# Optimization experiments

Hardware: AMD Instinct MI355X
Metric: run time of the kernel (lower is better)

## Reference

```python
import jax, jax.numpy as jnp
import numpy as np

DIM, HEADS, WS, SHIFT = 192, 6, 8, 4
HEAD_DIM = DIM // HEADS
SCALE = HEAD_DIM ** -0.5
EPS = 1e-5


def _rel_pos_index(ws):
    coords = np.stack(np.meshgrid(np.arange(ws), np.arange(ws), indexing='ij'))  # [2,ws,ws]
    flat = coords.reshape(2, -1)
    rel = flat[:, :, None] - flat[:, None, :]          # [2,N,N]
    rel = rel.transpose(1, 2, 0)
    rel[:, :, 0] += ws - 1
    rel[:, :, 1] += ws - 1
    rel[:, :, 0] *= 2 * ws - 1
    return rel.sum(-1)                                  # [N,N] int


def _attn_mask(H, W, ws, shift):
    if shift == 0:
        return None
    img = np.zeros((H, W), dtype=np.float32)
    cnt = 0
    for hs in (slice(0, -ws), slice(-ws, -shift), slice(-shift, None)):
        for wsl in (slice(0, -ws), slice(-ws, -shift), slice(-shift, None)):
            img[hs, wsl] = cnt
            cnt += 1
    mw = img.reshape(H // ws, ws, W // ws, ws).transpose(0, 2, 1, 3).reshape(-1, ws * ws)  # [nW,N]
    m = mw[:, None, :] - mw[:, :, None]
    return jnp.asarray(np.where(m != 0, -100.0, 0.0).astype(np.float32))  # [nW,N,N]


def _ln(x, w, b):
    mu = x.mean(-1, keepdims=True)
    var = ((x - mu) ** 2).mean(-1, keepdims=True)
    return (x - mu) * jax.lax.rsqrt(var + EPS) * w + b


def setup_inputs() -> dict:
    key = jax.random.key(0)
    ks = jax.random.split(key, 10)
    B, H, W, C = 64, 56, 56, DIM
    hid = 4 * C
    p = lambda k, sh, s=0.02: jax.random.normal(k, sh, jnp.float32) * s
    return {
        'x': jax.random.normal(ks[0], (B, H * W, C), jnp.float32),
        'ln1_w': jnp.ones((C,), jnp.float32), 'ln1_b': jnp.zeros((C,), jnp.float32),
        'qkv_w': p(ks[1], (C, 3 * C)), 'qkv_b': jnp.zeros((3 * C,), jnp.float32),
        'proj_w': p(ks[2], (C, C)), 'proj_b': jnp.zeros((C,), jnp.float32),
        'rpb_table': p(ks[3], ((2 * WS - 1) ** 2, HEADS)),
        'ln2_w': jnp.ones((C,), jnp.float32), 'ln2_b': jnp.zeros((C,), jnp.float32),
        'fc1_w': p(ks[4], (C, hid)), 'fc1_b': jnp.zeros((hid,), jnp.float32),
        'fc2_w': p(ks[5], (hid, C)), 'fc2_b': jnp.zeros((C,), jnp.float32),
        'H': H, 'W': W,
    }


def reference(x, ln1_w, ln1_b, qkv_w, qkv_b, proj_w, proj_b, rpb_table,
              ln2_w, ln2_b, fc1_w, fc1_b, fc2_w, fc2_b, H, W):
    B, L, C = x.shape
    N = WS * WS
    shortcut = x
    xn = _ln(x, ln1_w, ln1_b).reshape(B, H, W, C)
    xn = jnp.roll(xn, (-SHIFT, -SHIFT), (1, 2))
    # window partition -> [B*nW, N, C]
    xw = xn.reshape(B, H // WS, WS, W // WS, WS, C).transpose(0, 1, 3, 2, 4, 5)
    xw = xw.reshape(-1, N, C)
    B_ = xw.shape[0]
    qkv = (xw @ qkv_w + qkv_b).reshape(B_, N, 3, HEADS, HEAD_DIM).transpose(2, 0, 3, 1, 4)
    q, k, v = qkv[0], qkv[1], qkv[2]                    # [B_,h,N,d]
    attn = jnp.einsum('bhnd,bhmd->bhnm', q * SCALE, k)
    bias = rpb_table[_rel_pos_index(WS).reshape(-1)].reshape(N, N, HEADS).transpose(2, 0, 1)
    attn = attn + bias[None]
    mask = _attn_mask(H, W, WS, SHIFT)
    if mask is not None:
        nW = mask.shape[0]
        attn = attn.reshape(B_ // nW, nW, HEADS, N, N) + mask[None, :, None]
        attn = attn.reshape(B_, HEADS, N, N)
    attn = jax.nn.softmax(attn, axis=-1)
    out = jnp.einsum('bhnm,bhmd->bhnd', attn, v).transpose(0, 2, 1, 3).reshape(B_, N, C)
    out = out @ proj_w + proj_b
    # window reverse
    out = out.reshape(B, H // WS, W // WS, WS, WS, C).transpose(0, 1, 3, 2, 4, 5).reshape(B, H, W, C)
    out = jnp.roll(out, (SHIFT, SHIFT), (1, 2))
    x = shortcut + out.reshape(B, L, C)
    h = jax.nn.gelu(_ln(x, ln2_w, ln2_b) @ fc1_w + fc1_b, approximate=False)
    return x + (h @ fc2_w + fc2_b)
```

## Files before the change

### kernel.cpp

```cpp
#include <hip/hip_runtime.h>
#include <cstdint>
#include <cstddef>

#define WS_ 8
#define DIM_ 192
#define HEADS_ 6
#define HD_ 32
#define HH_ 56
#define NW_ 7
#define NWIN_ 49
#define LTOK_ 3136
#define NTOK_ 200704
#define NWTOT_ 3136
#define SHIFT_ 4
#define SCALE_ 0.17677669529663687f

typedef unsigned short ushort_t;
typedef __attribute__((ext_vector_type(8))) short short8;
typedef __attribute__((ext_vector_type(4))) short bf16x4;
typedef __attribute__((ext_vector_type(4))) float floatx4;
typedef __attribute__((ext_vector_type(8))) unsigned short ushort8;

__device__ __forceinline__ float b2f(ushort_t u) {
    union { unsigned int i; float f; } c; c.i = ((unsigned int)u) << 16; return c.f;
}
__device__ __forceinline__ ushort_t f2b(float f) {
    union { float f; unsigned int i; } c; c.f = f;
    unsigned int u = c.i;
    unsigned int r = (u + 0x7FFFu + ((u >> 16) & 1u)) >> 16;
    return (ushort_t)r;
}

__device__ __forceinline__ void load_lds16(const void* g, void* l) {
    __builtin_amdgcn_global_load_lds(
        (const __attribute__((address_space(1))) unsigned int*)g,
        (__attribute__((address_space(3))) unsigned int*)l, 16, 0, 0);
}

__device__ __forceinline__ int win_row_to_img(int r) {
    int win = r >> 6, n = r & 63;
    int b = win / NWIN_, wI = win - b * NWIN_;
    int wh = wI / NW_, wwi = wI - wh * NW_;
    int i = n >> 3, j = n & 7;
    int hh = wh * WS_ + i + SHIFT_; if (hh >= HH_) hh -= HH_;
    int ww = wwi * WS_ + j + SHIFT_; if (ww >= HH_) ww -= HH_;
    return b * LTOK_ + hh * HH_ + ww;
}

__global__ void transpose_kernel(const float* __restrict__ in,
                                 ushort_t* __restrict__ out, int K, int N) {
    int id = blockIdx.x * 256 + threadIdx.x;
    if (id >= K * N) return;
    int k = id / N, n = id - k * N;
    out[(size_t)n * K + k] = f2b(in[id]);
}

__global__ void bias_kernel(const float* __restrict__ rpb, float* __restrict__ Spre) {
    int th = blockIdx.x;
    int type = th / HEADS_, head = th - type * HEADS_;
    for (int idx = threadIdx.x; idx < 4096; idx += 256) {
        int q = idx >> 6, k = idx & 63;
        int i1 = q >> 3, j1 = q & 7, i2 = k >> 3, j2 = k & 7;
        int rel = (i1 - i2 + 7) * 15 + (j1 - j2 + 7);
        float v = rpb[rel * HEADS_ + head];
        int rh1 = (type & 2) ? (i1 < 4 ? 1 : 2) : 0;
        int rw1 = (type & 1) ? (j1 < 4 ? 1 : 2) : 0;
        int rh2 = (type & 2) ? (i2 < 4 ? 1 : 2) : 0;
        int rw2 = (type & 1) ? (j2 < 4 ? 1 : 2) : 0;
        if (rh1 != rh2 || rw1 != rw2) v -= 100.0f;
        Spre[(size_t)th * 4096 + idx] = v;
    }
}

template <bool PERMUTE>
__global__ __launch_bounds__(256) void ln_kernel(const float* __restrict__ xin,
                                                 const float* __restrict__ w,
                                                 const float* __restrict__ bia,
                                                 ushort_t* __restrict__ out,
                                                 int rowOff) {
    int t = blockIdx.x * 4 + (threadIdx.x >> 6);
    int lane = threadIdx.x & 63;
    int src = PERMUTE ? win_row_to_img(rowOff + t) : t;
    const float* xp = xin + (size_t)src * DIM_;
    float v0 = xp[lane];
    float v1 = xp[lane + 64];
    float v2 = xp[lane + 128];
    float s = v0 + v1 + v2;
    float ss = v0 * v0 + v1 * v1 + v2 * v2;
#pragma unroll
    for (int o = 32; o > 0; o >>= 1) {
        s += __shfl_xor(s, o);
        ss += __shfl_xor(ss, o);
    }
    float mu = s * (1.0f / 192.0f);
    float var = ss * (1.0f / 192.0f) - mu * mu;
    float inv = rsqrtf(var + 1e-5f);
    ushort_t* op = out + (size_t)t * DIM_;
    op[lane]       = f2b((v0 - mu) * inv * w[lane]       + bia[lane]);
    op[lane + 64]  = f2b((v1 - mu) * inv * w[lane + 64]  + bia[lane + 64]);
    op[lane + 128] = f2b((v2 - mu) * inv * w[lane + 128] + bia[lane + 128]);
}

#define EPI_STORE 0
#define EPI_GELU 1
#define EPI_PROJ 2
#define EPI_FC2 3
#define EPI_QKV 4

template <int EPI>
__global__ __launch_bounds__(256) void gemm_kernel(const ushort_t* __restrict__ A,
                                                   const ushort_t* __restrict__ Bt,
                                                   const float* __restrict__ bias,
                                                   void* __restrict__ outv,
                                                   const float* __restrict__ aux,
                                                   int K, int N, int rowOff) {
    __shared__ char smem[40960];

    int tid = threadIdx.x;
    int wave = tid >> 6, lane = tid & 63;
    int quad = lane >> 4, l16 = lane & 15;
    int wave_r = wave >> 1, wave_c = wave & 1;
    int row0 = blockIdx.x * 128;
    int n0 = blockIdx.y * 192;

    floatx4 acc[4][6];
#pragma unroll
    for (int rt = 0; rt < 4; ++rt)
#pragma unroll
        for (int ct = 0; ct < 6; ++ct)
#pragma unroll
            for (int e = 0; e < 4; ++e) acc[rt][ct][e] = 0.0f;

    int nk = K >> 5;

    auto stage = [&](int kk, int buf) {
#pragma unroll
        for (int j = 0; j < 2; ++j) {
            int o = (tid + j * 256) * 16;
            int row = o >> 6, kb = o & 63;
            const ushort_t* g = A + (size_t)(row0 + row) * K + kk * 32 + (kb >> 1);
            load_lds16(g, smem + buf * 8192 + o);
        }
#pragma unroll
        for (int j = 0; j < 3; ++j) {
            int o = (tid + j * 256) * 16;
            int row = o >> 6, kb = o & 63;
            const ushort_t* g = Bt + (size_t)(n0 + row) * K + kk * 32 + (kb >> 1);
            load_lds16(g, smem + 16384 + buf * 12288 + o);
        }
    };

    stage(0, 0);
    for (int kk = 0; kk < nk; ++kk) {
        int cur = kk & 1;
        __syncthreads();
        if (kk + 1 < nk) stage(kk + 1, cur ^ 1);

        short8 a[4];
#pragma unroll
        for (int rt = 0; rt < 4; ++rt)
            a[rt] = *(const short8*)(smem + cur * 8192 +
                     ((wave_r * 64 + rt * 16 + l16) * 64 + quad * 16));
#pragma unroll
        for (int ct = 0; ct < 6; ++ct) {
            short8 b = *(const short8*)(smem + 16384 + cur * 12288 +
                        ((wave_c * 96 + ct * 16 + l16) * 64 + quad * 16));
#pragma unroll
            for (int rt = 0; rt < 4; ++rt)
                acc[rt][ct] = __builtin_amdgcn_mfma_f32_16x16x32_bf16(a[rt], b, acc[rt][ct], 0, 0, 0);
        }
    }

#pragma unroll
    for (int ct = 0; ct < 6; ++ct) {
        int c = n0 + wave_c * 96 + ct * 16 + l16;
        float bs = bias[c];
#pragma unroll
        for (int rt = 0; rt < 4; ++rt) {
#pragma unroll
            for (int r = 0; r < 4; ++r) {
                int rr = row0 + wave_r * 64 + rt * 16 + quad * 4 + r;
                float val = acc[rt][ct][r] + bs;
                if (EPI == EPI_STORE) {
                    ((ushort_t*)outv)[(size_t)rr * N + c] = f2b(val);
                } else if (EPI == EPI_QKV) {
                    float sv = (c < DIM_) ? val * SCALE_ : val;
                    ((ushort_t*)outv)[(size_t)rr * N + c] = f2b(sv);
                } else if (EPI == EPI_GELU) {
                    float g = 0.5f * val * (1.0f + erff(val * 0.70710678118654752f));
                    ((ushort_t*)outv)[(size_t)rr * N + c] = f2b(g);
                } else if (EPI == EPI_PROJ) {
                    int dst = win_row_to_img(rowOff + rr);
                    size_t idx = (size_t)dst * DIM_ + c;
                    ((float*)outv)[idx] = val + aux[idx];
                } else {
                    size_t idx = (size_t)rr * DIM_ + c;
                    ((float*)outv)[idx] = val + aux[idx];
                }
            }
        }
    }
}

__global__ __launch_bounds__(256) void attn_kernel(const ushort_t* __restrict__ qkv,
                                                   const float* __restrict__ Spre,
                                                   ushort_t* __restrict__ aout,
                                                   int win0, int nwh) {
    __shared__ char smem[32768];
    int wave = threadIdx.x >> 6;
    int whid = blockIdx.x * 4 + wave;
    if (whid >= nwh) return;
    int lane = threadIdx.x & 63;
    int l16 = lane & 15, quad = lane >> 4;
    int winl = whid / HEADS_, head = whid - winl * HEADS_;
    int wI = (win0 + winl) % NWIN_;
    int wh = wI / NW_, wwi = wI - wh * NW_;
    int type = ((wh == 6) ? 2 : 0) + ((wwi == 6) ? 1 : 0);

    const ushort_t* qb = qkv + (size_t)(winl * 64) * 576 + head * HD_;

    short8 vfrag[2][2];
#pragma unroll
    for (int kk = 0; kk < 2; ++kk)
#pragma unroll
        for (int dt = 0; dt < 2; ++dt)
#pragma unroll
            for (int e = 0; e < 8; ++e)
                vfrag[dt][kk][e] =
                    (short)qb[(size_t)(kk * 32 + quad * 8 + e) * 576 + 2 * DIM_ + dt * 16 + l16];

    short8 kf[4], qf[4];
#pragma unroll
    for (int t = 0; t < 4; ++t) {
        kf[t] = *(const short8*)(qb + (size_t)(t * 16 + l16) * 576 + DIM_ + quad * 8);
        qf[t] = *(const short8*)(qb + (size_t)(t * 16 + l16) * 576 + quad * 8);
    }

    const float* bp = Spre + (size_t)(type * HEADS_ + head) * 4096;
    floatx4 acc[4][4];
#pragma unroll
    for (int art = 0; art < 4; ++art)
#pragma unroll
        for (int act = 0; act < 4; ++act)
            acc[art][act] = *(const floatx4*)(bp + (act * 16 + l16) * 64 + art * 16 + quad * 4);

#pragma unroll
    for (int art = 0; art < 4; ++art)
#pragma unroll
        for (int act = 0; act < 4; ++act)
            acc[art][act] = __builtin_amdgcn_mfma_f32_16x16x32_bf16(
                kf[art], qf[act], acc[art][act], 0, 0, 0);

    char* pb = smem + wave * 8192;
    int sw = (l16 & 7) << 4;
#pragma unroll
    for (int act = 0; act < 4; ++act) {
        float m = -1e30f;
#pragma unroll
        for (int art = 0; art < 4; ++art)
#pragma unroll
            for (int r = 0; r < 4; ++r) m = fmaxf(m, acc[art][act][r]);
        m = fmaxf(m, __shfl_xor(m, 16));
        m = fmaxf(m, __shfl_xor(m, 32));
        float s = 0.0f;
#pragma unroll
        for (int art = 0; art < 4; ++art)
#pragma unroll
            for (int r = 0; r < 4; ++r) {
                float e = __expf(acc[art][act][r] - m);
                acc[art][act][r] = e;
                s += e;
            }
        s += __shfl_xor(s, 16);
        s += __shfl_xor(s, 32);
        float inv = 1.0f / s;
        int q = act * 16 + l16;
        char* rowp = pb + q * 128;
#pragma unroll
        for (int art = 0; art < 4; ++art) {
            bf16x4 pk4;
#pragma unroll
            for (int r = 0; r < 4; ++r) pk4[r] = (short)f2b(acc[art][act][r] * inv);
            *(bf16x4*)(rowp + ((art * 32 + quad * 8) ^ sw)) = pk4;
        }
    }

    floatx4 accO[4][2];
#pragma unroll
    for (int ot = 0; ot < 4; ++ot)
#pragma unroll
        for (int dt = 0; dt < 2; ++dt)
#pragma unroll
            for (int e = 0; e < 4; ++e) accO[ot][dt][e] = 0.0f;
#pragma unroll
    for (int kk = 0; kk < 2; ++kk) {
        short8 pa[4];
#pragma unroll
        for (int ot = 0; ot < 4; ++ot)
            pa[ot] = *(const short8*)(pb + (ot * 16 + l16) * 128 +
                                      ((kk * 64 + quad * 16) ^ sw));
#pragma unroll
        for (int dt = 0; dt < 2; ++dt)
#pragma unroll
            for (int ot = 0; ot < 4; ++ot)
                accO[ot][dt] = __builtin_amdgcn_mfma_f32_16x16x32_bf16(
                    pa[ot], vfrag[dt][kk], accO[ot][dt], 0, 0, 0);
    }

    ushort_t* op = aout + (size_t)(winl * 64) * DIM_ + head * HD_;
#pragma unroll
    for (int ot = 0; ot < 4; ++ot)
#pragma unroll
        for (int dt = 0; dt < 2; ++dt)
#pragma unroll
            for (int r = 0; r < 4; ++r)
                op[(size_t)(ot * 16 + quad * 4 + r) * DIM_ + dt * 16 + l16] =
                    f2b(accO[ot][dt][r]);
}

extern "C" void kernel_launch(void* const* d_in, const int* in_sizes, int n_in,
                              void* d_out, int out_size, void* d_ws, size_t ws_size,
                              hipStream_t stream) {
    const float* x      = (const float*)d_in[0];
    const float* ln1_w  = (const float*)d_in[1];
    const float* ln1_b  = (const float*)d_in[2];
    const float* qkv_w  = (const float*)d_in[3];
    const float* qkv_b  = (const float*)d_in[4];
    const float* proj_w = (const float*)d_in[5];
    const float* proj_b = (const float*)d_in[6];
    const float* rpb    = (const float*)d_in[7];
    const float* ln2_w  = (const float*)d_in[8];
    const float* ln2_b  = (const float*)d_in[9];
    const float* fc1_w  = (const float*)d_in[10];
    const float* fc1_b  = (const float*)d_in[11];
    const float* fc2_w  = (const float*)d_in[12];
    const float* fc2_b  = (const float*)d_in[13];

    char* ws = (char*)d_ws;
    size_t off = 0;
    auto alloc = [&](size_t bytes) -> void* {
        void* p = ws + off;
        off += (bytes + 255) & ~(size_t)255;
        return p;
    };
    ushort_t* qkv_wt  = (ushort_t*)alloc((size_t)576 * 192 * 2);
    ushort_t* proj_wt = (ushort_t*)alloc((size_t)192 * 192 * 2);
    ushort_t* fc1_wt  = (ushort_t*)alloc((size_t)768 * 192 * 2);
    ushort_t* fc2_wt  = (ushort_t*)alloc((size_t)192 * 768 * 2);
    float*    SpreT   = (float*)alloc((size_t)4 * HEADS_ * 4096 * sizeof(float));

    float* x1 = (float*)d_out;

    size_t budget = (ws_size > off + 4096) ? (ws_size - off - 4096) : 0;
    long rows = (long)(budget / 1920);
    rows = (rows / 128) * 128;
    if (rows < 128) rows = 128;
    if (rows > NTOK_) rows = NTOK_;
    int chunkRows = (int)rows;
    int Wc = chunkRows / 64;
    if (Wc > NWTOT_) Wc = NWTOT_;

    ushort_t* bufS = (ushort_t*)alloc((size_t)chunkRows * 192 * 2);
    ushort_t* bufL = (ushort_t*)alloc((size_t)chunkRows * 768 * 2);
    (void)n_in; (void)in_sizes; (void)out_size;

    transpose_kernel<<<(192 * 576 + 255) / 256, 256, 0, stream>>>(qkv_w, qkv_wt, 192, 576);
    transpose_kernel<<<(192 * 192 + 255) / 256, 256, 0, stream>>>(proj_w, proj_wt, 192, 192);
    transpose_kernel<<<(192 * 768 + 255) / 256, 256, 0, stream>>>(fc1_w, fc1_wt, 192, 768);
    transpose_kernel<<<(768 * 192 + 255) / 256, 256, 0, stream>>>(fc2_w, fc2_wt, 768, 192);
    bias_kernel<<<4 * HEADS_, 256, 0, stream>>>(rpb, SpreT);

    for (int w0 = 0; w0 < NWTOT_; w0 += Wc) {
        int wc = NWTOT_ - w0 < Wc ? NWTOT_ - w0 : Wc;
        int rowsA = wc * 64;
        ln_kernel<true><<<rowsA / 4, 256, 0, stream>>>(x, ln1_w, ln1_b, bufS, w0 * 64);
        dim3 gq(rowsA / 128, 576 / 192);
        gemm_kernel<EPI_QKV><<<gq, 256, 0, stream>>>(bufS, qkv_wt, qkv_b, bufL, nullptr, 192, 576, 0);
        int nwh = wc * HEADS_;
        attn_kernel<<<(nwh + 3) / 4, 256, 0, stream>>>(bufL, SpreT, bufS, w0, nwh);
        dim3 gp(rowsA / 128, 1);
        gemm_kernel<EPI_PROJ><<<gp, 256, 0, stream>>>(bufS, proj_wt, proj_b, x1, x, 192, 192, w0 * 64);
    }

    for (int t0 = 0; t0 < NTOK_; t0 += chunkRows) {
        int tc = NTOK_ - t0 < chunkRows ? NTOK_ - t0 : chunkRows;
        ln_kernel<false><<<tc / 4, 256, 0, stream>>>(x1 + (size_t)t0 * 192, ln2_w, ln2_b, bufS, 0);
        dim3 g1(tc / 128, 768 / 192);
        gemm_kernel<EPI_GELU><<<g1, 256, 0, stream>>>(bufS, fc1_wt, fc1_b, bufL, nullptr, 192, 768, 0);
        dim3 g2(tc / 128, 1);
        gemm_kernel<EPI_FC2><<<g2, 256, 0, stream>>>(bufL, fc2_wt, fc2_b,
                                                     x1 + (size_t)t0 * 192,
                                                     x1 + (size_t)t0 * 192, 768, 192, 0);
    }
}
```

Measured before the change: 1.033 ms.

## Fuse LN2, FC1+GELU and FC2 into a single MLP kernel

Replaces the chunked LN2 / FC1-GELU / FC2 launch loop with one kernel per 64-token tile. The kernel normalizes rows into swizzled LDS, computes the hidden activations in two 384-wide halves kept in LDS, and accumulates FC2 in registers before adding the residual. This removes the global round trips of the normalized and 768-wide hidden buffers and many kernel launches. In exchange it uses 72KB of LDS per block, which limits occupancy, and weights are reloaded from global memory with no LDS staging.

```diff
diff --git a/kernel.cpp b/kernel.cpp
--- a/kernel.cpp
+++ b/kernel.cpp
@@ -318,6 +318,143 @@
                     f2b(accO[ot][dt][r]);
 }
 
+__global__ __launch_bounds__(256) void mlp_kernel(const float* __restrict__ x1,
+                                                  const float* __restrict__ lnw,
+                                                  const float* __restrict__ lnb,
+                                                  const ushort_t* __restrict__ w1t,
+                                                  const float* __restrict__ b1,
+                                                  const ushort_t* __restrict__ w2t,
+                                                  const float* __restrict__ b2,
+                                                  float* __restrict__ out) {
+    __shared__ char smem[24576 + 49152];
+    char* As = smem;
+    char* Hs = smem + 24576;
+    int tid = threadIdx.x;
+    int wave = tid >> 6, lane = tid & 63;
+    int quad = lane >> 4, l16 = lane & 15;
+    int row0 = blockIdx.x * 64;
+
+    {
+        float wa = lnw[lane], wb = lnw[lane + 64], wc2 = lnw[lane + 128];
+        float ba = lnb[lane], bb = lnb[lane + 64], bc2 = lnb[lane + 128];
+        for (int i = 0; i < 16; ++i) {
+            int row = i * 4 + wave;
+            const float* xp = x1 + (size_t)(row0 + row) * DIM_;
+            float v0 = xp[lane], v1 = xp[lane + 64], v2 = xp[lane + 128];
+            float s = v0 + v1 + v2;
+            float ss = v0 * v0 + v1 * v1 + v2 * v2;
+#pragma unroll
+            for (int o = 32; o > 0; o >>= 1) {
+                s += __shfl_xor(s, o);
+                ss += __shfl_xor(ss, o);
+            }
+            float mu = s * (1.0f / 192.0f);
+            float var = ss * (1.0f / 192.0f) - mu * mu;
+            float inv = rsqrtf(var + 1e-5f);
+            char* rp = As + row * 384;
+            int sx = (row & 7) << 4;
+            *(ushort_t*)(rp + ((lane * 2) ^ sx))         = f2b((v0 - mu) * inv * wa + ba);
+            *(ushort_t*)(rp + (((lane + 64) * 2) ^ sx))  = f2b((v1 - mu) * inv * wb + bb);
+            *(ushort_t*)(rp + (((lane + 128) * 2) ^ sx)) = f2b((v2 - mu) * inv * wc2 + bc2);
+        }
+    }
+    __syncthreads();
+
+    floatx4 acc2[4][3];
+#pragma unroll
+    for (int rt = 0; rt < 4; ++rt)
+#pragma unroll
+        for (int ct = 0; ct < 3; ++ct)
+#pragma unroll
+            for (int e = 0; e < 4; ++e) acc2[rt][ct][e] = 0.0f;
+
+#pragma unroll
+    for (int h = 0; h < 2; ++h) {
+#pragma unroll
+        for (int sub = 0; sub < 2; ++sub) {
+            floatx4 acc1[4][3];
+#pragma unroll
+            for (int rt = 0; rt < 4; ++rt)
+#pragma unroll
+                for (int ct = 0; ct < 3; ++ct)
+#pragma unroll
+                    for (int e = 0; e < 4; ++e) acc1[rt][ct][e] = 0.0f;
+#pragma unroll
+            for (int kk = 0; kk < 6; ++kk) {
+                short8 a[4];
+#pragma unroll
+                for (int rt = 0; rt < 4; ++rt) {
+                    int row = rt * 16 + l16;
+                    a[rt] = *(const short8*)(As + row * 384 +
+                             ((kk * 64 + quad * 16) ^ ((row & 7) << 4)));
+                }
+#pragma unroll
+                for (int ct = 0; ct < 3; ++ct) {
+                    int n = h * 384 + wave * 96 + sub * 48 + ct * 16 + l16;
+                    short8 bfr = *(const short8*)(w1t + (size_t)n * 192 + kk * 32 + quad * 8);
+#pragma unroll
+                    for (int rt = 0; rt < 4; ++rt)
+                        acc1[rt][ct] = __builtin_amdgcn_mfma_f32_16x16x32_bf16(
+                            a[rt], bfr, acc1[rt][ct], 0, 0, 0);
+                }
+            }
+#pragma unroll
+            for (int ct = 0; ct < 3; ++ct) {
+                int colh = wave * 96 + sub * 48 + ct * 16 + l16;
+                float bs = b1[h * 384 + colh];
+#pragma unroll
+                for (int rt = 0; rt < 4; ++rt) {
+#pragma unroll
+                    for (int r = 0; r < 4; ++r) {
+                        int row = rt * 16 + quad * 4 + r;
+                        float val = acc1[rt][ct][r] + bs;
+                        float g = 0.5f * val * (1.0f + erff(val * 0.70710678118654752f));
+                        *(ushort_t*)(Hs + row * 768 +
+                                     ((colh * 2) ^ ((row & 7) << 4))) = f2b(g);
+                    }
+                }
+            }
+        }
+        __syncthreads();
+#pragma unroll
+        for (int kk = 0; kk < 12; ++kk) {
+            short8 a[4];
+#pragma unroll
+            for (int rt = 0; rt < 4; ++rt) {
+                int row = rt * 16 + l16;
+                a[rt] = *(const short8*)(Hs + row * 768 +
+                         ((kk * 64 + quad * 16) ^ ((row & 7) << 4)));
+            }
+#pragma unroll
+            for (int ct = 0; ct < 3; ++ct) {
+                int n2 = wave * 48 + ct * 16 + l16;
+                short8 bfr = *(const short8*)(w2t + (size_t)n2 * 768 +
+                                              h * 384 + kk * 32 + quad * 8);
+#pragma unroll
+                for (int rt = 0; rt < 4; ++rt)
+                    acc2[rt][ct] = __builtin_amdgcn_mfma_f32_16x16x32_bf16(
+                        a[rt], bfr, acc2[rt][ct], 0, 0, 0);
+            }
+        }
+        __syncthreads();
+    }
+
+#pragma unroll
+    for (int ct = 0; ct < 3; ++ct) {
+        int c = wave * 48 + ct * 16 + l16;
+        float bs = b2[c];
+#pragma unroll
+        for (int rt = 0; rt < 4; ++rt) {
+#pragma unroll
+            for (int r = 0; r < 4; ++r) {
+                int rr = row0 + rt * 16 + quad * 4 + r;
+                size_t idx = (size_t)rr * DIM_ + c;
+                out[idx] = acc2[rt][ct][r] + bs + x1[idx];
+            }
+        }
+    }
+}
+
 extern "C" void kernel_launch(void* const* d_in, const int* in_sizes, int n_in,
                               void* d_out, int out_size, void* d_ws, size_t ws_size,
                               hipStream_t stream) {
@@ -382,14 +519,6 @@
         gemm_kernel<EPI_PROJ><<<gp, 256, 0, stream>>>(bufS, proj_wt, proj_b, x1, x, 192, 192, w0 * 64);
     }
 
-    for (int t0 = 0; t0 < NTOK_; t0 += chunkRows) {
-        int tc = NTOK_ - t0 < chunkRows ? NTOK_ - t0 : chunkRows;
-        ln_kernel<false><<<tc / 4, 256, 0, stream>>>(x1 + (size_t)t0 * 192, ln2_w, ln2_b, bufS, 0);
-        dim3 g1(tc / 128, 768 / 192);
-        gemm_kernel<EPI_GELU><<<g1, 256, 0, stream>>>(bufS, fc1_wt, fc1_b, bufL, nullptr, 192, 768, 0);
-        dim3 g2(tc / 128, 1);
-        gemm_kernel<EPI_FC2><<<g2, 256, 0, stream>>>(bufL, fc2_wt, fc2_b,
-                                                     x1 + (size_t)t0 * 192,
-                                                     x1 + (size_t)t0 * 192, 768, 192, 0);
-    }
-}
+    mlp_kernel<<<NTOK_ / 64, 256, 0, stream>>>(x1, ln2_w, ln2_b, fc1_wt, fc1_b,
+                                               fc2_wt, fc2_b, x1);
+}
```

New measurement: 1.267 ms. +22.7%, slower.
